# Optimization experiments

Hardware: AMD Instinct MI355X
Metric: run time of the kernel (lower is better)

## Reference

```python
import jax, jax.numpy as jnp
import numpy as np

N = 100000
E = 1600000
F_IN = 128
HID = 64
N_CLS = 16


def gcn_conv(x, row, col, W, b, n_nodes):
    # x: [N, Fin]; row/col: [E+N] (self-loops already appended)
    h = x @ W  # [N, Fout]
    ones = jnp.ones(row.shape[0], dtype=x.dtype)
    deg = jax.ops.segment_sum(ones, col, num_segments=n_nodes)  # in-degree incl. self-loop
    dinv = jnp.where(deg > 0, jax.lax.rsqrt(deg), 0.0)
    norm = dinv[row] * dinv[col]  # [E+N]
    msg = h[row] * norm[:, None]  # gather + scale
    out = jax.ops.segment_sum(msg, col, num_segments=n_nodes)  # scatter-add
    return out + b


def setup_inputs() -> dict:
    key = jax.random.key(0)
    k1, k2, k3, k4, k5, k6 = jax.random.split(key, 6)
    x = jax.random.normal(k1, (N, F_IN), dtype=jnp.float32)
    edge_index = jax.random.randint(k2, (2, E), 0, N, dtype=jnp.int64)
    # Glorot-ish init for weights
    W1 = jax.random.normal(k3, (F_IN, HID), dtype=jnp.float32) / np.sqrt(F_IN)
    b1 = jnp.zeros((HID,), dtype=jnp.float32)
    W2 = jax.random.normal(k4, (HID, N_CLS), dtype=jnp.float32) / np.sqrt(HID)
    b2 = jnp.zeros((N_CLS,), dtype=jnp.float32)
    return {"x": x, "edge_index": edge_index, "W1": W1, "b1": b1, "W2": W2, "b2": b2}


def reference(x, edge_index, W1, b1, W2, b2):
    # Add self-loops (GCNConv default add_self_loops=True)
    loop = jnp.arange(N, dtype=edge_index.dtype)
    row = jnp.concatenate([edge_index[0], loop])
    col = jnp.concatenate([edge_index[1], loop])
    h = gcn_conv(x, row, col, W1, b1, N)
    h = jax.nn.relu(h)
    h = gcn_conv(h, row, col, W2, b2, N)
    return jax.nn.log_softmax(h, axis=1)
```

## Files before the change

### kernel.cpp

```cpp
#include <hip/hip_runtime.h>
#include <hip/hip_fp16.h>

#define F_IN 128
#define HID  64
#define NCLS 16
#define NPB  128
#define CAP  4096
#define CHUNK 4096
#define W1PAD 136

typedef _Float16 half_t;
typedef __attribute__((ext_vector_type(8))) _Float16 half8;
typedef __attribute__((ext_vector_type(4))) float float4v;


__global__ __launch_bounds__(256) void bin_gemm(
    const int* __restrict__ row, const int* __restrict__ col,
    const float* __restrict__ x, const float* __restrict__ W1,
    int* __restrict__ cursor, int* __restrict__ ebuf,
    __half* __restrict__ hs1, int N, int E, int NB, int nbin)
{
    __shared__ __align__(16) char smem[17408];
    int t = threadIdx.x;

    if ((int)blockIdx.x < nbin) {
        int* hist = (int*)smem;
        int* base = (int*)smem + 1024;
        int* off  = (int*)smem + 2048;
        for (int i = t; i < NB; i += 256) hist[i] = 0;
        int base_e = blockIdx.x * CHUNK;
        int4 c4[4], r4[4];
        int nv[4];
        #pragma unroll
        for (int j = 0; j < 4; ++j) {
            int ej = base_e + j * 1024 + t * 4;
            int n = min(max(E - ej, 0), 4);
            nv[j] = n;
            c4[j] = make_int4(0, 0, 0, 0); r4[j] = make_int4(0, 0, 0, 0);
            if (n == 4) {
                c4[j] = *(const int4*)&col[ej];
                r4[j] = *(const int4*)&row[ej];
            } else {
                if (n > 0) { c4[j].x = col[ej + 0]; r4[j].x = row[ej + 0]; }
                if (n > 1) { c4[j].y = col[ej + 1]; r4[j].y = row[ej + 1]; }
                if (n > 2) { c4[j].z = col[ej + 2]; r4[j].z = row[ej + 2]; }
            }
        }
        __syncthreads();
        #pragma unroll
        for (int j = 0; j < 4; ++j) {
            if (nv[j] > 0) atomicAdd(&hist[c4[j].x >> 7], 1);
            if (nv[j] > 1) atomicAdd(&hist[c4[j].y >> 7], 1);
            if (nv[j] > 2) atomicAdd(&hist[c4[j].z >> 7], 1);
            if (nv[j] > 3) atomicAdd(&hist[c4[j].w >> 7], 1);
        }
        __syncthreads();
        for (int i = t; i < NB; i += 256) {
            int h = hist[i];
            base[i] = h ? (i * CAP + atomicAdd(&cursor[i], h)) : 0;
            off[i] = 0;
        }
        __syncthreads();
        #pragma unroll
        for (int j = 0; j < 4; ++j) {
            if (nv[j] > 0) { int b = c4[j].x >> 7; int p = base[b] + atomicAdd(&off[b], 1);
                             if (p < (b + 1) * CAP) ebuf[p] = (r4[j].x << 7) | (c4[j].x & (NPB - 1)); }
            if (nv[j] > 1) { int b = c4[j].y >> 7; int p = base[b] + atomicAdd(&off[b], 1);
                             if (p < (b + 1) * CAP) ebuf[p] = (r4[j].y << 7) | (c4[j].y & (NPB - 1)); }
            if (nv[j] > 2) { int b = c4[j].z >> 7; int p = base[b] + atomicAdd(&off[b], 1);
                             if (p < (b + 1) * CAP) ebuf[p] = (r4[j].z << 7) | (c4[j].z & (NPB - 1)); }
            if (nv[j] > 3) { int b = c4[j].w >> 7; int p = base[b] + atomicAdd(&off[b], 1);
                             if (p < (b + 1) * CAP) ebuf[p] = (r4[j].w << 7) | (c4[j].w & (NPB - 1)); }
        }
        return;
    }

    half_t* W1l = (half_t*)smem;
    for (int i = t; i < F_IN * HID; i += 256) {
        int k = i >> 6, n = i & 63;
        W1l[n * W1PAD + k] = (half_t)W1[i];
    }
    __syncthreads();

    int b = blockIdx.x - nbin;
    int node0 = b << 7;
    int wv = t >> 6, lane = t & 63;
    int l15 = lane & 15, quad = lane >> 4;
    int mbase = wv * 32;
    int r0 = min(node0 + mbase + l15, N - 1);
    int r1 = min(node0 + mbase + 16 + l15, N - 1);
    const float* x0 = x + (size_t)r0 * F_IN;
    const float* x1 = x + (size_t)r1 * F_IN;
    float4v acc[2][4];
    #pragma unroll
    for (int mt = 0; mt < 2; ++mt)
        #pragma unroll
        for (int j = 0; j < 4; ++j) acc[mt][j] = (float4v){0.f, 0.f, 0.f, 0.f};
    #pragma unroll
    for (int kb = 0; kb < 4; ++kb) {
        int off = kb * 32 + quad * 8;
        float4 fa = *(const float4*)&x0[off];
        float4 fb = *(const float4*)&x0[off + 4];
        float4 ga = *(const float4*)&x1[off];
        float4 gb = *(const float4*)&x1[off + 4];
        half8 a0 = {(half_t)fa.x, (half_t)fa.y, (half_t)fa.z, (half_t)fa.w,
                    (half_t)fb.x, (half_t)fb.y, (half_t)fb.z, (half_t)fb.w};
        half8 a1 = {(half_t)ga.x, (half_t)ga.y, (half_t)ga.z, (half_t)ga.w,
                    (half_t)gb.x, (half_t)gb.y, (half_t)gb.z, (half_t)gb.w};
        #pragma unroll
        for (int j = 0; j < 4; ++j) {
            half8 bv = *(const half8*)&W1l[(j * 16 + l15) * W1PAD + off];
            acc[0][j] = __builtin_amdgcn_mfma_f32_16x16x32_f16(a0, bv, acc[0][j], 0, 0, 0);
            acc[1][j] = __builtin_amdgcn_mfma_f32_16x16x32_f16(a1, bv, acc[1][j], 0, 0, 0);
        }
    }
    #pragma unroll
    for (int mt = 0; mt < 2; ++mt)
        #pragma unroll
        for (int j = 0; j < 4; ++j)
            #pragma unroll
            for (int r = 0; r < 4; ++r) {
                int m = mbase + mt * 16 + quad * 4 + r;
                int nn = node0 + m;
                if (nn < N) hs1[(size_t)nn * HID + j * 16 + l15] =
                    __float2half(acc[mt][j][r]);
            }
}


__global__ __launch_bounds__(256) void csr_scale(
    const int* __restrict__ ebuf, const int* __restrict__ cursor,
    int2* __restrict__ rsc, int* __restrict__ csr_row,
    __half* __restrict__ hs1, int N)
{
    __shared__ int hist[NPB];
    __shared__ float dv[NPB];
    __shared__ int cur[NPB];
    __shared__ int wtot;
    int t = threadIdx.x;
    int b = blockIdx.x;
    int node0 = b << 7;
    int ebase = b * CAP;

    int p[8];
    #pragma unroll
    for (int k = 0; k < 8; ++k) p[k] = ebuf[ebase + t + 256 * k];
    int cnt = min(cursor[b], CAP);
    if (t < NPB) hist[t] = 0;
    __syncthreads();
    #pragma unroll
    for (int k = 0; k < 8; ++k)
        if (t + 256 * k < cnt) atomicAdd(&hist[p[k] & (NPB - 1)], 1);
    if (cnt > 2048)
        for (int e = 2048 + t; e < cnt; e += 256)
            atomicAdd(&hist[ebuf[ebase + e] & (NPB - 1)], 1);
    __syncthreads();

    int h = 0, incl = 0;
    if (t < NPB) {
        h = hist[t];
        incl = h;
        #pragma unroll
        for (int off = 1; off < 64; off <<= 1) {
            int u = __shfl_up(incl, off, 64);
            if ((t & 63) >= off) incl += u;
        }
        if (t == 63) wtot = incl;
        dv[t] = rsqrtf((float)h + 1.0f);
    }
    __syncthreads();
    if (t < NPB) {
        if (t >= 64) incl += wtot;
        int start = ebase + incl - h;
        cur[t] = start;
        int n = node0 + t;
        if (n < N) rsc[n] = make_int2(start, h);
    }
    __syncthreads();

    #pragma unroll
    for (int k = 0; k < 8; ++k)
        if (t + 256 * k < cnt) {
            int pos = atomicAdd(&cur[p[k] & (NPB - 1)], 1);
            csr_row[pos] = p[k] >> 7;
        }
    if (cnt > 2048)
        for (int e = 2048 + t; e < cnt; e += 256) {
            int pp = ebuf[ebase + e];
            int pos = atomicAdd(&cur[pp & (NPB - 1)], 1);
            csr_row[pos] = pp >> 7;
        }

    half8* H = (half8*)hs1;
    for (int i = t; i < 1024; i += 256) {
        int r = i >> 3, s8 = i & 7;
        int n = node0 + r;
        if (n < N) {
            half8 v = H[(size_t)n * 8 + s8];
            float d = dv[r];
            #pragma unroll
            for (int k = 0; k < 8; ++k) v[k] = (half_t)((float)v[k] * d);
            H[(size_t)n * 8 + s8] = v;
        }
    }
}


__global__ __launch_bounds__(256) void agg_l1(
    const __half* __restrict__ hs1, const int2* __restrict__ rsc,
    const int* __restrict__ csr, const float* __restrict__ b1,
    const float* __restrict__ W2, __half* __restrict__ h2s, int N)
{
    __shared__ float W2l[HID * NCLS];
    __shared__ float o1[32][65];
    for (int i = threadIdx.x; i < HID * NCLS; i += 256) W2l[i] = W2[i];
    __syncthreads();
    int w = threadIdx.x >> 6, lane = threadIdx.x & 63;
    int g = lane >> 3, gl = lane & 7;
    int rowi = w * 8 + g;
    int c = blockIdx.x * 32 + rowi;
    bool active = (c < N);
    int cc = active ? c : 0;
    int2 rc = rsc[cc];
    int e0 = rc.x, e1 = rc.x + rc.y;
    float dc = rsqrtf((float)rc.y + 1.0f);
    const half8* H = (const half8*)hs1;
    half8 sv = H[(size_t)cc * 8 + gl];
    float sum[8];
    #pragma unroll
    for (int k = 0; k < 8; ++k) sum[k] = (float)sv[k];
    int i = e0;
    for (; i + 8 <= e1; i += 8) {
        int id[8];
        #pragma unroll
        for (int s = 0; s < 8; ++s) id[s] = csr[i + s];
        half8 a[8];
        #pragma unroll
        for (int s = 0; s < 8; ++s) a[s] = H[(size_t)id[s] * 8 + gl];
        half8 t0 = a[0] + a[1];
        half8 t1 = a[2] + a[3];
        half8 t2 = a[4] + a[5];
        half8 t3 = a[6] + a[7];
        half8 v = (t0 + t1) + (t2 + t3);
        #pragma unroll
        for (int k = 0; k < 8; ++k) sum[k] += (float)v[k];
    }
    if (i < e1) {
        int e1m1 = e1 - 1;
        int id[8];
        #pragma unroll
        for (int s = 0; s < 8; ++s) id[s] = csr[min(i + s, e1m1)];
        half8 a[8];
        #pragma unroll
        for (int s = 0; s < 8; ++s) a[s] = H[(size_t)id[s] * 8 + gl];
        #pragma unroll
        for (int s = 0; s < 8; ++s) {
            float fm = (i + s < e1) ? 1.f : 0.f;
            #pragma unroll
            for (int k = 0; k < 8; ++k) sum[k] = fmaf(fm, (float)a[s][k], sum[k]);
        }
    }
    float4 bb0 = *(const float4*)&b1[gl * 8];
    float4 bb1 = *(const float4*)&b1[gl * 8 + 4];
    o1[rowi][gl * 8 + 0] = fmaxf(fmaf(dc, sum[0], bb0.x), 0.f);
    o1[rowi][gl * 8 + 1] = fmaxf(fmaf(dc, sum[1], bb0.y), 0.f);
    o1[rowi][gl * 8 + 2] = fmaxf(fmaf(dc, sum[2], bb0.z), 0.f);
    o1[rowi][gl * 8 + 3] = fmaxf(fmaf(dc, sum[3], bb0.w), 0.f);
    o1[rowi][gl * 8 + 4] = fmaxf(fmaf(dc, sum[4], bb1.x), 0.f);
    o1[rowi][gl * 8 + 5] = fmaxf(fmaf(dc, sum[5], bb1.y), 0.f);
    o1[rowi][gl * 8 + 6] = fmaxf(fmaf(dc, sum[6], bb1.z), 0.f);
    o1[rowi][gl * 8 + 7] = fmaxf(fmaf(dc, sum[7], bb1.w), 0.f);
    int j0 = gl * 2, j1 = gl * 2 + 1;
    float s0 = 0.f, s1 = 0.f;
    const float* orow = o1[rowi];
    #pragma unroll 8
    for (int k = 0; k < HID; ++k) {
        float ov = orow[k];
        s0 = fmaf(ov, W2l[k * NCLS + j0], s0);
        s1 = fmaf(ov, W2l[k * NCLS + j1], s1);
    }
    if (active) {
        __half2 hv;
        hv.x = __float2half(dc * s0);
        hv.y = __float2half(dc * s1);
        ((__half2*)h2s)[(size_t)c * 8 + gl] = hv;
    }
}


__global__ __launch_bounds__(256) void agg2_final(
    const __half* __restrict__ h2s, const int2* __restrict__ rsc,
    const int* __restrict__ csr, const float* __restrict__ b2,
    float* __restrict__ out, int N)
{
    int t = threadIdx.x;
    int w = t >> 6, lane = t & 63;
    int nw = lane >> 1, hl = lane & 1;
    int c = blockIdx.x * 128 + w * 32 + nw;
    bool active = (c < N);
    int cc = active ? c : 0;
    int2 rc = rsc[cc];
    int e0 = rc.x, e1 = rc.x + rc.y;
    float dcv = rsqrtf((float)rc.y + 1.0f);
    const half8* H = (const half8*)h2s;
    half8 sv = H[(size_t)cc * 2 + hl];
    float sum[8];
    #pragma unroll
    for (int k = 0; k < 8; ++k) sum[k] = (float)sv[k];
    int i = e0;
    for (; i + 8 <= e1; i += 8) {
        int id[8];
        #pragma unroll
        for (int s = 0; s < 8; ++s) id[s] = csr[i + s];
        half8 a[8];
        #pragma unroll
        for (int s = 0; s < 8; ++s) a[s] = H[(size_t)id[s] * 2 + hl];
        half8 t0 = a[0] + a[1];
        half8 t1 = a[2] + a[3];
        half8 t2 = a[4] + a[5];
        half8 t3 = a[6] + a[7];
        half8 v = (t0 + t1) + (t2 + t3);
        #pragma unroll
        for (int k = 0; k < 8; ++k) sum[k] += (float)v[k];
    }
    if (i < e1) {
        int e1m1 = e1 - 1;
        int id[8];
        #pragma unroll
        for (int s = 0; s < 8; ++s) id[s] = csr[min(i + s, e1m1)];
        half8 a[8];
        #pragma unroll
        for (int s = 0; s < 8; ++s) a[s] = H[(size_t)id[s] * 2 + hl];
        #pragma unroll
        for (int s = 0; s < 8; ++s) {
            float fm = (i + s < e1) ? 1.f : 0.f;
            #pragma unroll
            for (int k = 0; k < 8; ++k) sum[k] = fmaf(fm, (float)a[s][k], sum[k]);
        }
    }
    float4 bb0 = *(const float4*)&b2[hl * 8];
    float4 bb1 = *(const float4*)&b2[hl * 8 + 4];
    float v0 = fmaf(dcv, sum[0], bb0.x);
    float v1 = fmaf(dcv, sum[1], bb0.y);
    float v2 = fmaf(dcv, sum[2], bb0.z);
    float v3 = fmaf(dcv, sum[3], bb0.w);
    float v4 = fmaf(dcv, sum[4], bb1.x);
    float v5 = fmaf(dcv, sum[5], bb1.y);
    float v6 = fmaf(dcv, sum[6], bb1.z);
    float v7 = fmaf(dcv, sum[7], bb1.w);
    float mx = fmaxf(fmaxf(fmaxf(v0, v1), fmaxf(v2, v3)),
                     fmaxf(fmaxf(v4, v5), fmaxf(v6, v7)));
    mx = fmaxf(mx, __shfl_xor(mx, 1, 64));
    float s = __expf(v0 - mx) + __expf(v1 - mx) + __expf(v2 - mx) + __expf(v3 - mx)
            + __expf(v4 - mx) + __expf(v5 - mx) + __expf(v6 - mx) + __expf(v7 - mx);
    s += __shfl_xor(s, 1, 64);
    float lse = mx + __logf(s);
    if (active) {
        float* o = out + (size_t)c * NCLS + hl * 8;
        *(float4*)&o[0] = make_float4(v0 - lse, v1 - lse, v2 - lse, v3 - lse);
        *(float4*)&o[4] = make_float4(v4 - lse, v5 - lse, v6 - lse, v7 - lse);
    }
}


extern "C" void kernel_launch(void* const* d_in, const int* in_sizes, int n_in,
                              void* d_out, int out_size, void* d_ws, size_t ws_size,
                              hipStream_t stream) {
    const float* x  = (const float*)d_in[0];
    const int*   ei = (const int*)d_in[1];
    const float* W1 = (const float*)d_in[2];
    const float* b1 = (const float*)d_in[3];
    const float* W2 = (const float*)d_in[4];
    const float* b2 = (const float*)d_in[5];
    float* out = (float*)d_out;

    const int N = in_sizes[0] / F_IN;
    const int E = in_sizes[1] / 2;
    const int* row = ei;
    const int* col = ei + E;

    const int NB = (N + NPB - 1) / NPB;
    size_t Np  = ((size_t)N + 15) & ~(size_t)15;
    size_t NBp = ((size_t)NB + 15) & ~(size_t)15;
    size_t Rg  = (size_t)NB * CAP;

    char* p = (char*)d_ws;
    __half* hs1     = (__half*)p;  p += Np * HID * 2;
    __half* h2s     = (__half*)p;  p += Np * NCLS * 2;
    int2*   rsc     = (int2*)p;    p += Np * 8;
    int*    csr_row = (int*)p;     p += Rg * 4;
    int*    ebuf    = (int*)p;     p += Rg * 4;
    int*    cursor  = (int*)p;     p += NBp * 4;

    int nbin = (E + CHUNK - 1) / CHUNK;

    hipMemsetAsync(cursor, 0, NBp * sizeof(int), stream);
    bin_gemm<<<nbin + NB, 256, 0, stream>>>(row, col, x, W1, cursor, ebuf,
                                            hs1, N, E, NB, nbin);
    csr_scale<<<NB, 256, 0, stream>>>(ebuf, cursor, rsc, csr_row, hs1, N);
    agg_l1<<<(N + 31) / 32, 256, 0, stream>>>(hs1, rsc, csr_row, b1, W2, h2s, N);
    agg2_final<<<(N + 127) / 128, 256, 0, stream>>>(h2s, rsc, csr_row, b2, out, N);
}
```

Baseline: 190.1 us.

## Enlarge binning chunk per block and pad global bin cursors to reduce atomic contention

Each binning block now processes 16384 edges in a two-pass loop (histogram pass, then re-read and scatter pass) instead of holding 4096 edges in registers. This cuts the number of global atomicAdds on the bin cursors by about four times. The cursors are also strided by 4 ints to spread them across cache lines. The trade-off is re-reading col/row from global memory in the second pass, plus fewer binning blocks running alongside the GEMM blocks.

```diff
diff --git a/kernel.cpp b/kernel.cpp
--- a/kernel.cpp
+++ b/kernel.cpp
@@ -6,8 +6,9 @@
 #define NCLS 16
 #define NPB  128
 #define CAP  4096
-#define CHUNK 4096
+#define CHUNK 16384
 #define W1PAD 136
+#define CSTRIDE 4
 
 typedef _Float16 half_t;
 typedef __attribute__((ext_vector_type(8))) _Float16 half8;
@@ -29,48 +30,50 @@
         int* off  = (int*)smem + 2048;
         for (int i = t; i < NB; i += 256) hist[i] = 0;
         int base_e = blockIdx.x * CHUNK;
-        int4 c4[4], r4[4];
-        int nv[4];
-        #pragma unroll
-        for (int j = 0; j < 4; ++j) {
-            int ej = base_e + j * 1024 + t * 4;
-            int n = min(max(E - ej, 0), 4);
-            nv[j] = n;
-            c4[j] = make_int4(0, 0, 0, 0); r4[j] = make_int4(0, 0, 0, 0);
-            if (n == 4) {
-                c4[j] = *(const int4*)&col[ej];
-                r4[j] = *(const int4*)&row[ej];
+        __syncthreads();
+        #pragma unroll 4
+        for (int s = 0; s < 16; ++s) {
+            int ej = base_e + s * 1024 + t * 4;
+            int nv = min(max(E - ej, 0), 4);
+            if (nv == 4) {
+                int4 c4 = *(const int4*)&col[ej];
+                atomicAdd(&hist[c4.x >> 7], 1);
+                atomicAdd(&hist[c4.y >> 7], 1);
+                atomicAdd(&hist[c4.z >> 7], 1);
+                atomicAdd(&hist[c4.w >> 7], 1);
             } else {
-                if (n > 0) { c4[j].x = col[ej + 0]; r4[j].x = row[ej + 0]; }
-                if (n > 1) { c4[j].y = col[ej + 1]; r4[j].y = row[ej + 1]; }
-                if (n > 2) { c4[j].z = col[ej + 2]; r4[j].z = row[ej + 2]; }
+                for (int q = ej; q < E; ++q) atomicAdd(&hist[col[q] >> 7], 1);
             }
-        }
-        __syncthreads();
-        #pragma unroll
-        for (int j = 0; j < 4; ++j) {
-            if (nv[j] > 0) atomicAdd(&hist[c4[j].x >> 7], 1);
-            if (nv[j] > 1) atomicAdd(&hist[c4[j].y >> 7], 1);
-            if (nv[j] > 2) atomicAdd(&hist[c4[j].z >> 7], 1);
-            if (nv[j] > 3) atomicAdd(&hist[c4[j].w >> 7], 1);
         }
         __syncthreads();
         for (int i = t; i < NB; i += 256) {
             int h = hist[i];
-            base[i] = h ? (i * CAP + atomicAdd(&cursor[i], h)) : 0;
+            base[i] = h ? (i * CAP + atomicAdd(&cursor[i * CSTRIDE], h)) : 0;
             off[i] = 0;
         }
         __syncthreads();
-        #pragma unroll
-        for (int j = 0; j < 4; ++j) {
-            if (nv[j] > 0) { int b = c4[j].x >> 7; int p = base[b] + atomicAdd(&off[b], 1);
-                             if (p < (b + 1) * CAP) ebuf[p] = (r4[j].x << 7) | (c4[j].x & (NPB - 1)); }
-            if (nv[j] > 1) { int b = c4[j].y >> 7; int p = base[b] + atomicAdd(&off[b], 1);
-                             if (p < (b + 1) * CAP) ebuf[p] = (r4[j].y << 7) | (c4[j].y & (NPB - 1)); }
-            if (nv[j] > 2) { int b = c4[j].z >> 7; int p = base[b] + atomicAdd(&off[b], 1);
-                             if (p < (b + 1) * CAP) ebuf[p] = (r4[j].z << 7) | (c4[j].z & (NPB - 1)); }
-            if (nv[j] > 3) { int b = c4[j].w >> 7; int p = base[b] + atomicAdd(&off[b], 1);
-                             if (p < (b + 1) * CAP) ebuf[p] = (r4[j].w << 7) | (c4[j].w & (NPB - 1)); }
+        #pragma unroll 4
+        for (int s = 0; s < 16; ++s) {
+            int ej = base_e + s * 1024 + t * 4;
+            int nv = min(max(E - ej, 0), 4);
+            if (nv == 4) {
+                int4 c4 = *(const int4*)&col[ej];
+                int4 r4 = *(const int4*)&row[ej];
+                int b0 = c4.x >> 7; int p0 = base[b0] + atomicAdd(&off[b0], 1);
+                if (p0 < (b0 + 1) * CAP) ebuf[p0] = (r4.x << 7) | (c4.x & (NPB - 1));
+                int b1 = c4.y >> 7; int p1 = base[b1] + atomicAdd(&off[b1], 1);
+                if (p1 < (b1 + 1) * CAP) ebuf[p1] = (r4.y << 7) | (c4.y & (NPB - 1));
+                int b2 = c4.z >> 7; int p2 = base[b2] + atomicAdd(&off[b2], 1);
+                if (p2 < (b2 + 1) * CAP) ebuf[p2] = (r4.z << 7) | (c4.z & (NPB - 1));
+                int b3 = c4.w >> 7; int p3 = base[b3] + atomicAdd(&off[b3], 1);
+                if (p3 < (b3 + 1) * CAP) ebuf[p3] = (r4.w << 7) | (c4.w & (NPB - 1));
+            } else {
+                for (int q = ej; q < E; ++q) {
+                    int c = col[q], b = c >> 7;
+                    int p = base[b] + atomicAdd(&off[b], 1);
+                    if (p < (b + 1) * CAP) ebuf[p] = (row[q] << 7) | (c & (NPB - 1));
+                }
+            }
         }
         return;
     }
@@ -145,7 +148,7 @@
     int p[8];
     #pragma unroll
     for (int k = 0; k < 8; ++k) p[k] = ebuf[ebase + t + 256 * k];
-    int cnt = min(cursor[b], CAP);
+    int cnt = min(cursor[b * CSTRIDE], CAP);
     if (t < NPB) hist[t] = 0;
     __syncthreads();
     #pragma unroll
@@ -390,11 +393,11 @@
     int2*   rsc     = (int2*)p;    p += Np * 8;
     int*    csr_row = (int*)p;     p += Rg * 4;
     int*    ebuf    = (int*)p;     p += Rg * 4;
-    int*    cursor  = (int*)p;     p += NBp * 4;
+    int*    cursor  = (int*)p;     p += NBp * 4 * CSTRIDE;
 
     int nbin = (E + CHUNK - 1) / CHUNK;
 
-    hipMemsetAsync(cursor, 0, NBp * sizeof(int), stream);
+    hipMemsetAsync(cursor, 0, NBp * sizeof(int) * CSTRIDE, stream);
     bin_gemm<<<nbin + NB, 256, 0, stream>>>(row, col, x, W1, cursor, ebuf,
                                             hs1, N, E, NB, nbin);
     csr_scale<<<NB, 256, 0, stream>>>(ebuf, cursor, rsc, csr_row, hs1, N);
```

Result: faster. 184.7 us (-2.8%).

## Drop hs1 prescale pass, apply dinv in aggregation, stage GEMM stores, prefetch indices

Applied to the files above, without the earlier changes.

The layer-1 GEMM output is now staged through shared memory so each row is written with coalesced 16-byte stores instead of scattered 2-byte stores. The separate read-modify-write pass in the CSR kernel that scaled hs1 by the degree normalisation is removed. Instead a dinv array is written, and agg_l1 gathers dinv per neighbour and applies it with FMAs. Both aggregation kernels also software-prefetch the next batch of CSR indices. This saves a full pass over hs1 but adds a random 4-byte gather per edge and replaces the half-precision pairwise adds with more fp32 FMAs.

```diff
diff --git a/kernel.cpp b/kernel.cpp
--- a/kernel.cpp
+++ b/kernel.cpp
@@ -8,6 +8,7 @@
 #define CAP  4096
 #define CHUNK 4096
 #define W1PAD 136
+#define SPAD 72
 
 typedef _Float16 half_t;
 typedef __attribute__((ext_vector_type(8))) _Float16 half8;
@@ -20,7 +21,7 @@
     int* __restrict__ cursor, int* __restrict__ ebuf,
     __half* __restrict__ hs1, int N, int E, int NB, int nbin)
 {
-    __shared__ __align__(16) char smem[17408];
+    __shared__ __align__(16) char smem[18432];
     int t = threadIdx.x;
 
     if ((int)blockIdx.x < nbin) {
@@ -114,6 +115,8 @@
             acc[1][j] = __builtin_amdgcn_mfma_f32_16x16x32_f16(a1, bv, acc[1][j], 0, 0, 0);
         }
     }
+    __syncthreads();
+    half_t* stage = (half_t*)smem;
     #pragma unroll
     for (int mt = 0; mt < 2; ++mt)
         #pragma unroll
@@ -121,20 +124,27 @@
             #pragma unroll
             for (int r = 0; r < 4; ++r) {
                 int m = mbase + mt * 16 + quad * 4 + r;
-                int nn = node0 + m;
-                if (nn < N) hs1[(size_t)nn * HID + j * 16 + l15] =
-                    __float2half(acc[mt][j][r]);
+                stage[m * SPAD + j * 16 + l15] = (half_t)acc[mt][j][r];
             }
+    __syncthreads();
+    #pragma unroll
+    for (int k = 0; k < 4; ++k) {
+        int i = t + 256 * k;
+        int rrow = i >> 3, seg = i & 7;
+        int n = node0 + rrow;
+        if (n < N)
+            *(half8*)&((half_t*)hs1)[(size_t)n * HID + seg * 8] =
+                *(const half8*)&stage[rrow * SPAD + seg * 8];
+    }
 }
 
 
-__global__ __launch_bounds__(256) void csr_scale(
+__global__ __launch_bounds__(256) void csr_dinv(
     const int* __restrict__ ebuf, const int* __restrict__ cursor,
     int2* __restrict__ rsc, int* __restrict__ csr_row,
-    __half* __restrict__ hs1, int N)
+    float* __restrict__ dinv, int N)
 {
     __shared__ int hist[NPB];
-    __shared__ float dv[NPB];
     __shared__ int cur[NPB];
     __shared__ int wtot;
     int t = threadIdx.x;
@@ -166,7 +176,6 @@
             if ((t & 63) >= off) incl += u;
         }
         if (t == 63) wtot = incl;
-        dv[t] = rsqrtf((float)h + 1.0f);
     }
     __syncthreads();
     if (t < NPB) {
@@ -174,10 +183,12 @@
         int start = ebase + incl - h;
         cur[t] = start;
         int n = node0 + t;
-        if (n < N) rsc[n] = make_int2(start, h);
-    }
-    __syncthreads();
-
+        if (n < N) {
+            rsc[n] = make_int2(start, h);
+            dinv[n] = rsqrtf((float)h + 1.0f);
+        }
+    }
+    __syncthreads();
     #pragma unroll
     for (int k = 0; k < 8; ++k)
         if (t + 256 * k < cnt) {
@@ -190,26 +201,14 @@
             int pos = atomicAdd(&cur[pp & (NPB - 1)], 1);
             csr_row[pos] = pp >> 7;
         }
-
-    half8* H = (half8*)hs1;
-    for (int i = t; i < 1024; i += 256) {
-        int r = i >> 3, s8 = i & 7;
-        int n = node0 + r;
-        if (n < N) {
-            half8 v = H[(size_t)n * 8 + s8];
-            float d = dv[r];
-            #pragma unroll
-            for (int k = 0; k < 8; ++k) v[k] = (half_t)((float)v[k] * d);
-            H[(size_t)n * 8 + s8] = v;
-        }
-    }
 }
 
 
 __global__ __launch_bounds__(256) void agg_l1(
     const __half* __restrict__ hs1, const int2* __restrict__ rsc,
-    const int* __restrict__ csr, const float* __restrict__ b1,
-    const float* __restrict__ W2, __half* __restrict__ h2s, int N)
+    const int* __restrict__ csr, const float* __restrict__ dinv,
+    const float* __restrict__ b1, const float* __restrict__ W2,
+    __half* __restrict__ h2s, int N)
 {
     __shared__ float W2l[HID * NCLS];
     __shared__ float o1[32][65];
@@ -228,37 +227,48 @@
     half8 sv = H[(size_t)cc * 8 + gl];
     float sum[8];
     #pragma unroll
-    for (int k = 0; k < 8; ++k) sum[k] = (float)sv[k];
-    int i = e0;
-    for (; i + 8 <= e1; i += 8) {
-        int id[8];
-        #pragma unroll
-        for (int s = 0; s < 8; ++s) id[s] = csr[i + s];
+    for (int k = 0; k < 8; ++k) sum[k] = dc * (float)sv[k];
+    int nfull = (e1 - e0) >> 3;
+    int id[8];
+    if (nfull > 0) {
+        #pragma unroll
+        for (int s = 0; s < 8; ++s) id[s] = csr[e0 + s];
+    }
+    for (int it = 0; it < nfull; ++it) {
         half8 a[8];
+        float dvr[8];
         #pragma unroll
         for (int s = 0; s < 8; ++s) a[s] = H[(size_t)id[s] * 8 + gl];
-        half8 t0 = a[0] + a[1];
-        half8 t1 = a[2] + a[3];
-        half8 t2 = a[4] + a[5];
-        half8 t3 = a[6] + a[7];
-        half8 v = (t0 + t1) + (t2 + t3);
-        #pragma unroll
-        for (int k = 0; k < 8; ++k) sum[k] += (float)v[k];
-    }
+        #pragma unroll
+        for (int s = 0; s < 8; ++s) dvr[s] = dinv[id[s]];
+        int ib = e0 + (it + 1) * 8;
+        if (it + 1 < nfull) {
+            #pragma unroll
+            for (int s = 0; s < 8; ++s) id[s] = csr[ib + s];
+        }
+        #pragma unroll
+        for (int s = 0; s < 8; ++s)
+            #pragma unroll
+            for (int k = 0; k < 8; ++k)
+                sum[k] = fmaf(dvr[s], (float)a[s][k], sum[k]);
+    }
+    int i = e0 + nfull * 8;
     if (i < e1) {
         int e1m1 = e1 - 1;
-        int id[8];
-        #pragma unroll
-        for (int s = 0; s < 8; ++s) id[s] = csr[min(i + s, e1m1)];
+        int idt[8];
+        #pragma unroll
+        for (int s = 0; s < 8; ++s) idt[s] = csr[min(i + s, e1m1)];
         half8 a[8];
-        #pragma unroll
-        for (int s = 0; s < 8; ++s) a[s] = H[(size_t)id[s] * 8 + gl];
-        #pragma unroll
-        for (int s = 0; s < 8; ++s) {
-            float fm = (i + s < e1) ? 1.f : 0.f;
-            #pragma unroll
-            for (int k = 0; k < 8; ++k) sum[k] = fmaf(fm, (float)a[s][k], sum[k]);
-        }
+        float dvr[8];
+        #pragma unroll
+        for (int s = 0; s < 8; ++s) a[s] = H[(size_t)idt[s] * 8 + gl];
+        #pragma unroll
+        for (int s = 0; s < 8; ++s) dvr[s] = (i + s < e1) ? dinv[idt[s]] : 0.f;
+        #pragma unroll
+        for (int s = 0; s < 8; ++s)
+            #pragma unroll
+            for (int k = 0; k < 8; ++k)
+                sum[k] = fmaf(dvr[s], (float)a[s][k], sum[k]);
     }
     float4 bb0 = *(const float4*)&b1[gl * 8];
     float4 bb1 = *(const float4*)&b1[gl * 8 + 4];
@@ -307,14 +317,21 @@
     float sum[8];
     #pragma unroll
     for (int k = 0; k < 8; ++k) sum[k] = (float)sv[k];
-    int i = e0;
-    for (; i + 8 <= e1; i += 8) {
-        int id[8];
-        #pragma unroll
-        for (int s = 0; s < 8; ++s) id[s] = csr[i + s];
+    int nfull = (e1 - e0) >> 3;
+    int id[8];
+    if (nfull > 0) {
+        #pragma unroll
+        for (int s = 0; s < 8; ++s) id[s] = csr[e0 + s];
+    }
+    for (int it = 0; it < nfull; ++it) {
         half8 a[8];
         #pragma unroll
         for (int s = 0; s < 8; ++s) a[s] = H[(size_t)id[s] * 2 + hl];
+        int ib = e0 + (it + 1) * 8;
+        if (it + 1 < nfull) {
+            #pragma unroll
+            for (int s = 0; s < 8; ++s) id[s] = csr[ib + s];
+        }
         half8 t0 = a[0] + a[1];
         half8 t1 = a[2] + a[3];
         half8 t2 = a[4] + a[5];
@@ -323,14 +340,15 @@
         #pragma unroll
         for (int k = 0; k < 8; ++k) sum[k] += (float)v[k];
     }
+    int i = e0 + nfull * 8;
     if (i < e1) {
         int e1m1 = e1 - 1;
-        int id[8];
-        #pragma unroll
-        for (int s = 0; s < 8; ++s) id[s] = csr[min(i + s, e1m1)];
+        int idt[8];
+        #pragma unroll
+        for (int s = 0; s < 8; ++s) idt[s] = csr[min(i + s, e1m1)];
         half8 a[8];
         #pragma unroll
-        for (int s = 0; s < 8; ++s) a[s] = H[(size_t)id[s] * 2 + hl];
+        for (int s = 0; s < 8; ++s) a[s] = H[(size_t)idt[s] * 2 + hl];
         #pragma unroll
         for (int s = 0; s < 8; ++s) {
             float fm = (i + s < e1) ? 1.f : 0.f;
@@ -387,6 +405,7 @@
     char* p = (char*)d_ws;
     __half* hs1     = (__half*)p;  p += Np * HID * 2;
     __half* h2s     = (__half*)p;  p += Np * NCLS * 2;
+    float*  dinv    = (float*)p;   p += Np * 4;
     int2*   rsc     = (int2*)p;    p += Np * 8;
     int*    csr_row = (int*)p;     p += Rg * 4;
     int*    ebuf    = (int*)p;     p += Rg * 4;
@@ -397,7 +416,7 @@
     hipMemsetAsync(cursor, 0, NBp * sizeof(int), stream);
     bin_gemm<<<nbin + NB, 256, 0, stream>>>(row, col, x, W1, cursor, ebuf,
                                             hs1, N, E, NB, nbin);
-    csr_scale<<<NB, 256, 0, stream>>>(ebuf, cursor, rsc, csr_row, hs1, N);
-    agg_l1<<<(N + 31) / 32, 256, 0, stream>>>(hs1, rsc, csr_row, b1, W2, h2s, N);
+    csr_dinv<<<NB, 256, 0, stream>>>(ebuf, cursor, rsc, csr_row, dinv, N);
+    agg_l1<<<(N + 31) / 32, 256, 0, stream>>>(hs1, rsc, csr_row, dinv, b1, W2, h2s, N);
     agg2_final<<<(N + 127) / 128, 256, 0, stream>>>(h2s, rsc, csr_row, b2, out, N);
 }
```

Result: no change. 188.7 us (-0.7%).
